# Kernel tuning notes

Measured on AMD Instinct MI355X. Metric: run time of the kernel, lower is better.

The kernel has to match this reference:

```python
import jax, jax.numpy as jnp
import numpy as np

N_RAYS = 131072
N_SAMPLES = 128
FEAT_DIM = 3
FAR_DELTA = 1e10  # sentinel delta appended for the last sample, as in the torch code


def setup_inputs() -> dict:
    key = jax.random.key(0)
    k1, k2, k3 = jax.random.split(key, 3)
    # densities are non-negative (output of e.g. relu/softplus in NeRF)
    density = jax.random.uniform(k1, (N_RAYS, N_SAMPLES), dtype=jnp.float32) * 2.0
    feature = jax.random.uniform(k2, (N_RAYS, N_SAMPLES, FEAT_DIM), dtype=jnp.float32)
    # monotonically increasing per-ray sample depths: near + cumsum(uniform bins)
    bins = jax.random.uniform(k3, (N_RAYS, N_SAMPLES), dtype=jnp.float32) * 0.05 + 0.01
    depth_values = 1.0 + jnp.cumsum(bins, axis=1)
    return {"density": density, "feature": feature, "depth_values": depth_values}


def reference(density, feature, depth_values):
    # deltas: consecutive depth differences, with a huge last delta (torch.cat(..., 1e10*ones))
    deltas = jnp.concatenate(
        [depth_values[:, 1:] - depth_values[:, :-1],
         jnp.full_like(depth_values[:, :1], FAR_DELTA)],
        axis=-1,
    )  # [N, S]
    att = jnp.exp(-density * deltas)              # exp(-sigma_i * delta_i), [N, S]
    # inclusive prefix product, matching the loop: T[i] = T[i-1]*exp(-sigma_i*delta_i)
    T = jnp.cumprod(att, axis=1)                  # [N, S]
    weights = T * (1.0 - att)                     # [N, S]
    feat_out = jnp.einsum("ns,nsc->nc", weights, feature)      # [N, 3]
    depth_out = jnp.sum(weights * depth_values, axis=1)         # [N]
    return feat_out, depth_out
```

## Files before the change

kernel.cpp:

```cpp
#include <hip/hip_runtime.h>

#define N_RAYS    131072
#define N_SAMPLES 128
#define FAR_DELTA 1e10f

__global__ __launch_bounds__(256) void VolumeRenderer_57612691308835_kernel(
    const float* __restrict__ density,
    const float* __restrict__ feature,
    const float* __restrict__ depth,
    float* __restrict__ out_feat,
    float* __restrict__ out_depth)
{
    const int wave = threadIdx.x >> 6;
    const int lane = threadIdx.x & 63;
    const int ray  = (blockIdx.x << 2) + wave;
    if (ray >= N_RAYS) return;

    const int  s0   = lane << 1;
    const long base = (long)ray * N_SAMPLES;

    const float2 den = *(const float2*)(density + base + s0);
    const float2 dep = *(const float2*)(depth   + base + s0);
    const float* fp  = feature + (base + s0) * 3;
    const float2 f01 = *(const float2*)(fp);
    const float2 f23 = *(const float2*)(fp + 2);
    const float2 f45 = *(const float2*)(fp + 4);

    const float d_next = __shfl_down(dep.x, 1);
    const float delta0 = dep.y - dep.x;
    const float delta1 = (lane == 63) ? FAR_DELTA : (d_next - dep.y);

    const float att0 = __expf(-den.x * delta0);
    const float att1 = __expf(-den.y * delta1);

    float scan = att0 * att1;
    #pragma unroll
    for (int off = 1; off < 64; off <<= 1) {
        const float v = __shfl_up(scan, off);
        scan *= (lane >= off) ? v : 1.0f;
    }
    float excl = __shfl_up(scan, 1);
    if (lane == 0) excl = 1.0f;

    const float T0 = excl * att0;
    const float T1 = T0   * att1;
    const float w0 = T0 * (1.0f - att0);
    const float w1 = T1 * (1.0f - att1);

    float fx = w0 * f01.x + w1 * f23.y;
    float fy = w0 * f01.y + w1 * f45.x;
    float fz = w0 * f23.x + w1 * f45.y;
    float dd = w0 * dep.x + w1 * dep.y;

    #pragma unroll
    for (int off = 32; off >= 1; off >>= 1) {
        fx += __shfl_xor(fx, off);
        fy += __shfl_xor(fy, off);
        fz += __shfl_xor(fz, off);
        dd += __shfl_xor(dd, off);
    }

    if (lane == 0) {
        out_feat[ray * 3 + 0] = fx;
        out_feat[ray * 3 + 1] = fy;
        out_feat[ray * 3 + 2] = fz;
        out_depth[ray]        = dd;
    }
}

extern "C" void kernel_launch(void* const* d_in, const int* in_sizes, int n_in,
                              void* d_out, int out_size, void* d_ws, size_t ws_size,
                              hipStream_t stream) {
    const float* density = (const float*)d_in[0];
    const float* feature = (const float*)d_in[1];
    const float* depth   = (const float*)d_in[2];

    float* out_feat  = (float*)d_out;
    float* out_depth = (float*)d_out + (long)N_RAYS * 3;

    const int rays_per_block = 4;
    const int grid = N_RAYS / rays_per_block;
    VolumeRenderer_57612691308835_kernel<<<grid, 256, 0, stream>>>(
        density, feature, depth, out_feat, out_depth);
}
```

Before: 351.3 us.

## Stage features through LDS with coalesced float4 loads and batch rays per wave

Each block now handles 16 rays, four per wave. The block's whole feature slab is copied into shared memory with coalesced float4 loads, and the strided per-lane reads are served from LDS. Density and depth loads for all four rays are issued up front, which raises the number of memory requests in flight. The cost is 24KB of LDS per block, a block-wide barrier, and more registers, all of which may limit occupancy.

```diff
diff --git a/kernel.cpp b/kernel.cpp
--- a/kernel.cpp
+++ b/kernel.cpp
@@ -3,6 +3,12 @@
 #define N_RAYS    131072
 #define N_SAMPLES 128
 #define FAR_DELTA 1e10f
+
+#define WAVES_PER_BLOCK 4
+#define RAYS_PER_WAVE   4
+#define RAYS_PER_BLOCK  (WAVES_PER_BLOCK * RAYS_PER_WAVE)
+#define FEAT_FLOATS     (N_SAMPLES * 3)
+#define LDS_FLOATS      (RAYS_PER_BLOCK * FEAT_FLOATS)
 
 __global__ __launch_bounds__(256) void VolumeRenderer_57612691308835_kernel(
     const float* __restrict__ density,
@@ -11,60 +17,88 @@
     float* __restrict__ out_feat,
     float* __restrict__ out_depth)
 {
-    const int wave = threadIdx.x >> 6;
-    const int lane = threadIdx.x & 63;
-    const int ray  = (blockIdx.x << 2) + wave;
-    if (ray >= N_RAYS) return;
+    __shared__ float lds_feat[LDS_FLOATS];
 
-    const int  s0   = lane << 1;
-    const long base = (long)ray * N_SAMPLES;
+    const int tid  = threadIdx.x;
+    const int wave = tid >> 6;
+    const int lane = tid & 63;
+    const int blockRay0 = blockIdx.x * RAYS_PER_BLOCK;
+    const int s0 = lane << 1;
 
-    const float2 den = *(const float2*)(density + base + s0);
-    const float2 dep = *(const float2*)(depth   + base + s0);
-    const float* fp  = feature + (base + s0) * 3;
-    const float2 f01 = *(const float2*)(fp);
-    const float2 f23 = *(const float2*)(fp + 2);
-    const float2 f45 = *(const float2*)(fp + 4);
+    float2 den[RAYS_PER_WAVE], dep[RAYS_PER_WAVE];
+    #pragma unroll
+    for (int r = 0; r < RAYS_PER_WAVE; ++r) {
+        const long base = (long)(blockRay0 + wave * RAYS_PER_WAVE + r) * N_SAMPLES;
+        den[r] = *(const float2*)(density + base + s0);
+        dep[r] = *(const float2*)(depth   + base + s0);
+    }
 
-    const float d_next = __shfl_down(dep.x, 1);
-    const float delta0 = dep.y - dep.x;
-    const float delta1 = (lane == 63) ? FAR_DELTA : (d_next - dep.y);
+    {
+        const float4* gsrc = (const float4*)(feature + (long)blockRay0 * FEAT_FLOATS);
+        float4* lds4 = (float4*)lds_feat;
+        #pragma unroll
+        for (int i = 0; i < LDS_FLOATS / 4 / 256; ++i)
+            lds4[tid + i * 256] = gsrc[tid + i * 256];
+    }
+    __syncthreads();
 
-    const float att0 = __expf(-den.x * delta0);
-    const float att1 = __expf(-den.y * delta1);
+    float fx[RAYS_PER_WAVE], fy[RAYS_PER_WAVE], fz[RAYS_PER_WAVE], dd[RAYS_PER_WAVE];
 
-    float scan = att0 * att1;
     #pragma unroll
-    for (int off = 1; off < 64; off <<= 1) {
-        const float v = __shfl_up(scan, off);
-        scan *= (lane >= off) ? v : 1.0f;
+    for (int r = 0; r < RAYS_PER_WAVE; ++r) {
+        const int rl = wave * RAYS_PER_WAVE + r;
+
+        const float* fp = lds_feat + rl * FEAT_FLOATS + s0 * 3;
+        const float f0 = fp[0], f1 = fp[1], f2 = fp[2];
+        const float f3 = fp[3], f4 = fp[4], f5 = fp[5];
+
+        const float d_next = __shfl_down(dep[r].x, 1);
+        const float delta0 = dep[r].y - dep[r].x;
+        const float delta1 = (lane == 63) ? FAR_DELTA : (d_next - dep[r].y);
+
+        const float att0 = __expf(-den[r].x * delta0);
+        const float att1 = __expf(-den[r].y * delta1);
+
+        float scan = att0 * att1;
+        #pragma unroll
+        for (int off = 1; off < 64; off <<= 1) {
+            const float v = __shfl_up(scan, off);
+            scan *= (lane >= off) ? v : 1.0f;
+        }
+        float excl = __shfl_up(scan, 1);
+        if (lane == 0) excl = 1.0f;
+
+        const float T0 = excl * att0;
+        const float T1 = T0   * att1;
+        const float w0 = T0 * (1.0f - att0);
+        const float w1 = T1 * (1.0f - att1);
+
+        fx[r] = w0 * f0 + w1 * f3;
+        fy[r] = w0 * f1 + w1 * f4;
+        fz[r] = w0 * f2 + w1 * f5;
+        dd[r] = w0 * dep[r].x + w1 * dep[r].y;
     }
-    float excl = __shfl_up(scan, 1);
-    if (lane == 0) excl = 1.0f;
-
-    const float T0 = excl * att0;
-    const float T1 = T0   * att1;
-    const float w0 = T0 * (1.0f - att0);
-    const float w1 = T1 * (1.0f - att1);
-
-    float fx = w0 * f01.x + w1 * f23.y;
-    float fy = w0 * f01.y + w1 * f45.x;
-    float fz = w0 * f23.x + w1 * f45.y;
-    float dd = w0 * dep.x + w1 * dep.y;
 
     #pragma unroll
     for (int off = 32; off >= 1; off >>= 1) {
-        fx += __shfl_xor(fx, off);
-        fy += __shfl_xor(fy, off);
-        fz += __shfl_xor(fz, off);
-        dd += __shfl_xor(dd, off);
+        #pragma unroll
+        for (int r = 0; r < RAYS_PER_WAVE; ++r) {
+            fx[r] += __shfl_xor(fx[r], off);
+            fy[r] += __shfl_xor(fy[r], off);
+            fz[r] += __shfl_xor(fz[r], off);
+            dd[r] += __shfl_xor(dd[r], off);
+        }
     }
 
     if (lane == 0) {
-        out_feat[ray * 3 + 0] = fx;
-        out_feat[ray * 3 + 1] = fy;
-        out_feat[ray * 3 + 2] = fz;
-        out_depth[ray]        = dd;
+        #pragma unroll
+        for (int r = 0; r < RAYS_PER_WAVE; ++r) {
+            const int ray = blockRay0 + wave * RAYS_PER_WAVE + r;
+            out_feat[ray * 3 + 0] = fx[r];
+            out_feat[ray * 3 + 1] = fy[r];
+            out_feat[ray * 3 + 2] = fz[r];
+            out_depth[ray]        = dd[r];
+        }
     }
 }
 
@@ -78,8 +112,7 @@
     float* out_feat  = (float*)d_out;
     float* out_depth = (float*)d_out + (long)N_RAYS * 3;
 
-    const int rays_per_block = 4;
-    const int grid = N_RAYS / rays_per_block;
+    const int grid = N_RAYS / RAYS_PER_BLOCK;
     VolumeRenderer_57612691308835_kernel<<<grid, 256, 0, stream>>>(
         density, feature, depth, out_feat, out_depth);
 }
```

New measurement: 360.1 us. +2.5%, slower.

## Process each ray with four threads doing sequential scans over vectorized loads

Applied to the files above, without the earlier changes.

Replaces the one-wave-per-ray layout with four threads per ray. Each thread loads 32 samples with float4 reads and computes a sequential local transmittance product and weighted sums. A small four-lane shuffle scan and reduction then combines the partial results. This removes most cross-lane shuffle work and the narrow 8-byte loads, at the cost of more registers per thread and strided per-thread memory access.

```diff
diff --git a/kernel.cpp b/kernel.cpp
--- a/kernel.cpp
+++ b/kernel.cpp
@@ -3,6 +3,10 @@
 #define N_RAYS    131072
 #define N_SAMPLES 128
 #define FAR_DELTA 1e10f
+
+#define THREADS_PER_RAY 4
+#define SAMPLES_PER_THREAD (N_SAMPLES / THREADS_PER_RAY)
+#define GROUPS 8
 
 __global__ __launch_bounds__(256) void VolumeRenderer_57612691308835_kernel(
     const float* __restrict__ density,
@@ -11,60 +15,76 @@
     float* __restrict__ out_feat,
     float* __restrict__ out_depth)
 {
-    const int wave = threadIdx.x >> 6;
-    const int lane = threadIdx.x & 63;
-    const int ray  = (blockIdx.x << 2) + wave;
-    if (ray >= N_RAYS) return;
+    const int gtid = blockIdx.x * 256 + threadIdx.x;
+    const int ray  = gtid >> 2;
+    const int sub  = gtid & 3;
 
-    const int  s0   = lane << 1;
-    const long base = (long)ray * N_SAMPLES;
+    const long sbase = (long)ray * N_SAMPLES + sub * SAMPLES_PER_THREAD;
+    const float4* __restrict__ dep4p = (const float4*)(depth   + sbase);
+    const float4* __restrict__ den4p = (const float4*)(density + sbase);
+    const float4* __restrict__ f4p   = (const float4*)(feature + sbase * 3);
 
-    const float2 den = *(const float2*)(density + base + s0);
-    const float2 dep = *(const float2*)(depth   + base + s0);
-    const float* fp  = feature + (base + s0) * 3;
-    const float2 f01 = *(const float2*)(fp);
-    const float2 f23 = *(const float2*)(fp + 2);
-    const float2 f45 = *(const float2*)(fp + 4);
+    const float4 dep_first = dep4p[0];
+    const float  next_depth = __shfl_down(dep_first.x, 1);
 
-    const float d_next = __shfl_down(dep.x, 1);
-    const float delta0 = dep.y - dep.x;
-    const float delta1 = (lane == 63) ? FAR_DELTA : (d_next - dep.y);
+    float Tloc = 1.0f;
+    float sfx = 0.f, sfy = 0.f, sfz = 0.f, sdd = 0.f;
 
-    const float att0 = __expf(-den.x * delta0);
-    const float att1 = __expf(-den.y * delta1);
+    float c_dep = 0.f, c_den = 0.f, c_f0 = 0.f, c_f1 = 0.f, c_f2 = 0.f;
 
-    float scan = att0 * att1;
-    #pragma unroll
-    for (int off = 1; off < 64; off <<= 1) {
-        const float v = __shfl_up(scan, off);
-        scan *= (lane >= off) ? v : 1.0f;
-    }
-    float excl = __shfl_up(scan, 1);
-    if (lane == 0) excl = 1.0f;
-
-    const float T0 = excl * att0;
-    const float T1 = T0   * att1;
-    const float w0 = T0 * (1.0f - att0);
-    const float w1 = T1 * (1.0f - att1);
-
-    float fx = w0 * f01.x + w1 * f23.y;
-    float fy = w0 * f01.y + w1 * f45.x;
-    float fz = w0 * f23.x + w1 * f45.y;
-    float dd = w0 * dep.x + w1 * dep.y;
+    auto process = [&](float den, float delta, float f0, float f1, float f2,
+                       float d) {
+        const float att = __expf(-den * delta);
+        Tloc *= att;
+        const float w = Tloc * (1.0f - att);
+        sfx += w * f0;
+        sfy += w * f1;
+        sfz += w * f2;
+        sdd += w * d;
+    };
 
     #pragma unroll
-    for (int off = 32; off >= 1; off >>= 1) {
-        fx += __shfl_xor(fx, off);
-        fy += __shfl_xor(fy, off);
-        fz += __shfl_xor(fz, off);
-        dd += __shfl_xor(dd, off);
+    for (int g = 0; g < GROUPS; ++g) {
+        const float4 dep4 = (g == 0) ? dep_first : dep4p[g];
+        const float4 den4 = den4p[g];
+        const float4 fA = f4p[3 * g + 0];
+        const float4 fB = f4p[3 * g + 1];
+        const float4 fC = f4p[3 * g + 2];
+
+        if (g > 0)
+            process(c_den, dep4.x - c_dep, c_f0, c_f1, c_f2, c_dep);
+
+        process(den4.x, dep4.y - dep4.x, fA.x, fA.y, fA.z, dep4.x);
+        process(den4.y, dep4.z - dep4.y, fA.w, fB.x, fB.y, dep4.y);
+        process(den4.z, dep4.w - dep4.z, fB.z, fB.w, fC.x, dep4.z);
+
+        c_dep = dep4.w; c_den = den4.w;
+        c_f0 = fC.y; c_f1 = fC.z; c_f2 = fC.w;
     }
 
-    if (lane == 0) {
-        out_feat[ray * 3 + 0] = fx;
-        out_feat[ray * 3 + 1] = fy;
-        out_feat[ray * 3 + 2] = fz;
-        out_depth[ray]        = dd;
+    {
+        const float delta = (sub == 3) ? FAR_DELTA : (next_depth - c_dep);
+        process(c_den, delta, c_f0, c_f1, c_f2, c_dep);
+    }
+
+    float p = Tloc;
+    float v = __shfl_up(p, 1); if (sub >= 1) p *= v;
+    v       = __shfl_up(p, 2); if (sub >= 2) p *= v;
+    float excl = __shfl_up(p, 1);
+    if (sub == 0) excl = 1.0f;
+
+    sfx *= excl; sfy *= excl; sfz *= excl; sdd *= excl;
+
+    sfx += __shfl_xor(sfx, 1); sfx += __shfl_xor(sfx, 2);
+    sfy += __shfl_xor(sfy, 1); sfy += __shfl_xor(sfy, 2);
+    sfz += __shfl_xor(sfz, 1); sfz += __shfl_xor(sfz, 2);
+    sdd += __shfl_xor(sdd, 1); sdd += __shfl_xor(sdd, 2);
+
+    if (sub == 0) {
+        out_feat[ray * 3 + 0] = sfx;
+        out_feat[ray * 3 + 1] = sfy;
+        out_feat[ray * 3 + 2] = sfz;
+        out_depth[ray]        = sdd;
     }
 }
 
@@ -78,8 +98,8 @@
     float* out_feat  = (float*)d_out;
     float* out_depth = (float*)d_out + (long)N_RAYS * 3;
 
-    const int rays_per_block = 4;
-    const int grid = N_RAYS / rays_per_block;
+    const int total_threads = N_RAYS * THREADS_PER_RAY;
+    const int grid = total_threads / 256;
     VolumeRenderer_57612691308835_kernel<<<grid, 256, 0, stream>>>(
         density, feature, depth, out_feat, out_depth);
 }
```

After: 412.4 us. 1.17x slower.
